# Kernel optimization log

Hardware: AMD Instinct MI355X
Metric: run time of the kernel (lower is better)

The kernel has to match this reference:

```python
import jax
jax.config.update("jax_enable_x64", True)
import jax.numpy as jnp
import numpy as np

# Paillier parameters (small primes so all modular arithmetic is exact in int64)
P, Q = 59, 61
N = P * Q                    # 3599, public modulus
N2 = N * N                   # 12,952,801; (N2-1)^2 < 2^63 -> int64-safe
LAM = (P - 1) * (Q - 1) // np.gcd(P - 1, Q - 1)   # lcm(p-1, q-1) = 870
MU = pow(int(LAM), -1, int(N))                     # lambda^{-1} mod n (g = n+1 variant)
LAM_BITS = [(LAM >> i) & 1 for i in range(int(LAM).bit_length())]  # LSB-first, static


def _decrypt(c):
    """Batched Paillier decryption: m = L(c^lambda mod n^2) * mu mod n, L(x)=(x-1)//n."""
    b = c % N2
    r = jnp.ones_like(b)
    # static square-and-multiply over the 10 bits of lambda (fully unrolled, elementwise)
    for bit in LAM_BITS:
        if bit:
            r = (r * b) % N2
        b = (b * b) % N2
    return ((r - 1) // N * MU) % N


def setup_inputs() -> dict:
    key = jax.random.key(0)
    k1, _ = jax.random.split(key)
    c = jax.random.randint(k1, (8192, 4096), 1, N2, dtype=jnp.int64)
    inv_scale = jnp.ones((1,), dtype=jnp.float32)
    return {"c": c, "inv_scale": inv_scale}


def reference(c, inv_scale):
    dec = _decrypt(c).astype(jnp.float32)
    # original: activation(decrypt(c) / 1000); inv_scale == 1.0 keeps math identical
    return jax.nn.relu(dec * (inv_scale / 1000.0))
```

## Files before the change

### kernel.cpp

```cpp
#include <hip/hip_runtime.h>
#include <stdint.h>

static constexpr uint32_t PP  = 59, QQ = 61;
static constexpr uint32_t Nn  = PP * QQ;
static constexpr uint32_t P2  = PP * PP;
static constexpr uint32_t Q2  = QQ * QQ;
static constexpr uint32_t LAM = 1740;

constexpr uint32_t cinv(uint32_t a, uint32_t m) {
    for (uint32_t x = 1; x < m; ++x) if ((uint64_t)a * x % m == 1u) return x;
    return 0u;
}
static constexpr uint32_t MU  = cinv(LAM % Nn, Nn);
static constexpr uint32_t IQP = cinv(P2 % Q2, Q2);
static constexpr uint32_t GAM = cinv(PP % QQ, QQ);
static constexpr uint32_t CPP = (cinv(QQ % PP, PP) * (MU % PP)) % PP;
static constexpr uint32_t CQQ = (cinv(PP % QQ, QQ) * (MU % QQ)) % QQ;

static constexpr int TPN = 3484;
static constexpr int TQN = 3724;
static constexpr int TT  = TPN + TQN;
static constexpr size_t WS_NEED = (size_t)TT * 4;

__device__ __forceinline__ uint32_t mul24lo(uint32_t a, uint32_t b) {
    uint32_t r;
    asm("v_mul_u32_u24 %0, %1, %2" : "=v"(r) : "v"(a), "v"(b));
    return r;
}
__device__ __forceinline__ uint32_t mul24hi(uint32_t a, uint32_t b) {
    uint32_t r;
    asm("v_mul_hi_u32_u24 %0, %1, %2" : "=v"(r) : "v"(a), "v"(b));
    return r;
}
__device__ __forceinline__ uint32_t mad24_59(uint32_t a, uint32_t c) {
    uint32_t r;
    asm("v_mad_u32_u24 %0, %1, 59, %2" : "=v"(r) : "v"(a), "v"(c));
    return r;
}

template<uint32_t D>
__device__ __forceinline__ uint32_t mod24(uint32_t x) {
    constexpr uint32_t M = (uint32_t)((1ull << 32) / D);
    uint32_t q = mul24hi(x, M);
    uint32_t r = x - mul24lo(q, D);
    return min(r, r - D);
}

template<uint32_t MOD>
__device__ uint32_t pow1740(uint32_t base) {
    uint32_t b = base % MOD, r = 1u, e = LAM;
    while (e) {
        if (e & 1u) r = (r * b) % MOD;
        b = (b * b) % MOD;
        e >>= 1u;
    }
    return r;
}
__device__ uint32_t m_from_r(uint32_t r) {
    if (r == 0u) return Nn - MU;
    uint32_t x = (r - 1u) / Nn;
    return (x * MU) % Nn;
}
__device__ uint32_t tp_entry(uint32_t i) {
    uint32_t a = pow1740<P2>(i);
    uint32_t flag = (i % PP == 0u) ? 0x80000000u : 0u;
    uint32_t gp = 0u, mp = 0u;
    if (!flag) {
        uint32_t s = (a - 1u) / PP;
        mp = (s * CPP) % PP;
        gp = (mp * GAM) % QQ;
    }
    uint32_t t = (uint32_t)(((uint64_t)((Q2 - a % Q2) % Q2) * IQP) % Q2);
    uint32_t r = a + P2 * t;
    uint32_t dq = m_from_r(r);
    return gp | (mp << 8) | (dq << 16) | flag;
}
__device__ uint32_t tq_entry(uint32_t i) {
    uint32_t b = pow1740<Q2>(i);
    uint32_t flag = (i % QQ == 0u) ? 0x80000000u : 0u;
    uint32_t gq = 0u;
    if (!flag) {
        uint32_t s = (b - 1u) / QQ;
        uint32_t mq = (s * CQQ) % QQ;
        gq = (mq * GAM) % QQ;
    }
    uint32_t t = (uint32_t)(((uint64_t)b * IQP) % Q2);
    uint32_t r = P2 * t;
    uint32_t dp = m_from_r(r);
    return gq | (dp << 16) | flag;
}

__global__ void build_tables(uint32_t* __restrict__ T) {
    int i = blockIdx.x * blockDim.x + threadIdx.x;
    if (i < TPN) T[i]       = (i < (int)P2) ? tp_entry((uint32_t)i) : 0u;
    if (i < TQN) T[TPN + i] = (i < (int)Q2) ? tq_entry((uint32_t)i) : 0u;
}

__device__ __forceinline__ float dec1(uint32_t c, const uint32_t* sTp,
                                      const uint32_t* sTq, float scale) {
    uint32_t up = sTp[mod24<P2>(c)];
    uint32_t uq = sTq[mod24<Q2>(c)];
    uint32_t gp  = up & 63u;
    uint32_t mp  = (up >> 8) & 63u;
    uint32_t dqv = (up >> 16) & 0xFFFu;
    uint32_t gq  = uq & 63u;
    uint32_t dpv = (uq >> 16) & 0xFFFu;
    uint32_t d = gq + QQ - gp;
    d = min(d, d - QQ);
    uint32_t m = mad24_59(d, mp);
    m = ((int32_t)uq < 0) ? dqv : m;
    m = ((int32_t)up < 0) ? dpv : m;
    return fmaxf((float)m * scale, 0.0f);
}

#define BLK 512

__global__ __launch_bounds__(BLK, 8) void paillier_main(
        const uint4* __restrict__ in4, float4* __restrict__ out,
        const uint32_t* __restrict__ T, const float* __restrict__ inv_scale,
        int n4) {
    __shared__ uint32_t sT[TT];
    for (int k = threadIdx.x; k < TT / 4; k += BLK)
        ((uint4*)sT)[k] = ((const uint4*)T)[k];
    __syncthreads();
    const uint32_t* sTp = sT;
    const uint32_t* sTq = sT + TPN;

    float scale = inv_scale[0] / 1000.0f;

    int stride = gridDim.x * BLK;
    for (int i = blockIdx.x * BLK + threadIdx.x; i < n4; i += stride) {
        uint4 a = in4[i];
        float4 o;
        o.x = dec1(a.x, sTp, sTq, scale);
        o.y = dec1(a.y, sTp, sTq, scale);
        o.z = dec1(a.z, sTp, sTq, scale);
        o.w = dec1(a.w, sTp, sTq, scale);
        out[i] = o;
    }
}

__global__ __launch_bounds__(BLK) void paillier_main_fb(
        const uint4* __restrict__ in4, float4* __restrict__ out,
        const float* __restrict__ inv_scale, int n4) {
    __shared__ uint32_t sT[TT];
    for (int i = threadIdx.x; i < (int)P2; i += BLK) sT[i]       = tp_entry((uint32_t)i);
    for (int i = threadIdx.x; i < (int)Q2; i += BLK) sT[TPN + i] = tq_entry((uint32_t)i);
    __syncthreads();
    const uint32_t* sTp = sT;
    const uint32_t* sTq = sT + TPN;
    float scale = inv_scale[0] / 1000.0f;
    int stride = gridDim.x * BLK;
    for (int i = blockIdx.x * BLK + threadIdx.x; i < n4; i += stride) {
        uint4 a = in4[i];
        float4 o;
        o.x = dec1(a.x, sTp, sTq, scale);
        o.y = dec1(a.y, sTp, sTq, scale);
        o.z = dec1(a.z, sTp, sTq, scale);
        o.w = dec1(a.w, sTp, sTq, scale);
        out[i] = o;
    }
}

extern "C" void kernel_launch(void* const* d_in, const int* in_sizes, int n_in,
                              void* d_out, int out_size, void* d_ws, size_t ws_size,
                              hipStream_t stream) {
    const uint4* c        = (const uint4*)d_in[0];
    const float* invscale = (const float*)d_in[1];
    float4* out           = (float4*)d_out;

    int n  = in_sizes[0];
    int n4 = n / 4;

    int nblk = 1024;
    int need = (n4 + BLK - 1) / BLK;
    if (nblk > need) nblk = need;

    if (ws_size >= WS_NEED && d_ws != nullptr) {
        uint32_t* T = (uint32_t*)d_ws;
        build_tables<<<(TQN + 255) / 256, 256, 0, stream>>>(T);
        paillier_main<<<nblk, BLK, 0, stream>>>(c, out, T, invscale, n4);
    } else {
        paillier_main_fb<<<nblk, BLK, 0, stream>>>(c, out, invscale, n4);
    }
}
```

Before: 235.3 us.

## Software-pipeline input loads four strides ahead and use nontemporal stores

The grid-stride decrypt loop is restructured so each thread holds four uint4 loads in flight and issues the next batch of four before decoding the current one. This is meant to hide global-memory latency in a bandwidth-bound streaming kernel. Output stores become nontemporal to reduce cache pollution. The extra live registers may lower occupancy under the 512x8 launch bounds.

New measurement: 240.6 us. +2.2%, slower.

```diff
diff --git a/kernel.cpp b/kernel.cpp
--- a/kernel.cpp
+++ b/kernel.cpp
@@ -113,7 +113,58 @@
     return fmaxf((float)m * scale, 0.0f);
 }
 
+__device__ __forceinline__ float4 dec4(uint4 a, const uint32_t* sTp,
+                                       const uint32_t* sTq, float scale) {
+    float4 o;
+    o.x = dec1(a.x, sTp, sTq, scale);
+    o.y = dec1(a.y, sTp, sTq, scale);
+    o.z = dec1(a.z, sTp, sTq, scale);
+    o.w = dec1(a.w, sTp, sTq, scale);
+    return o;
+}
+
+typedef float f32x4_t __attribute__((ext_vector_type(4)));
+__device__ __forceinline__ void st4(float4* __restrict__ out, int i, float4 o) {
+    f32x4_t v = {o.x, o.y, o.z, o.w};
+    __builtin_nontemporal_store(v, reinterpret_cast<f32x4_t*>(out + i));
+}
+
 #define BLK 512
+
+__device__ __forceinline__ void dec_loop(const uint4* __restrict__ in4,
+                                         float4* __restrict__ out,
+                                         const uint32_t* sTp, const uint32_t* sTq,
+                                         float scale, int n4) {
+    const int stride = gridDim.x * BLK;
+    int i = blockIdx.x * BLK + threadIdx.x;
+    if (i + 3 * stride < n4) {
+        uint4 a0 = in4[i];
+        uint4 a1 = in4[i + stride];
+        uint4 a2 = in4[i + 2 * stride];
+        uint4 a3 = in4[i + 3 * stride];
+        int j = i + 4 * stride;
+        while (j + 3 * stride < n4) {
+            uint4 b0 = in4[j];
+            uint4 b1 = in4[j + stride];
+            uint4 b2 = in4[j + 2 * stride];
+            uint4 b3 = in4[j + 3 * stride];
+            st4(out, i,              dec4(a0, sTp, sTq, scale));
+            st4(out, i + stride,     dec4(a1, sTp, sTq, scale));
+            st4(out, i + 2 * stride, dec4(a2, sTp, sTq, scale));
+            st4(out, i + 3 * stride, dec4(a3, sTp, sTq, scale));
+            a0 = b0; a1 = b1; a2 = b2; a3 = b3;
+            i = j; j += 4 * stride;
+        }
+        st4(out, i,              dec4(a0, sTp, sTq, scale));
+        st4(out, i + stride,     dec4(a1, sTp, sTq, scale));
+        st4(out, i + 2 * stride, dec4(a2, sTp, sTq, scale));
+        st4(out, i + 3 * stride, dec4(a3, sTp, sTq, scale));
+        i += 4 * stride;
+    }
+    for (; i < n4; i += stride) {
+        st4(out, i, dec4(in4[i], sTp, sTq, scale));
+    }
+}
 
 __global__ __launch_bounds__(BLK, 8) void paillier_main(
         const uint4* __restrict__ in4, float4* __restrict__ out,
@@ -127,17 +178,7 @@
     const uint32_t* sTq = sT + TPN;
 
     float scale = inv_scale[0] / 1000.0f;
-
-    int stride = gridDim.x * BLK;
-    for (int i = blockIdx.x * BLK + threadIdx.x; i < n4; i += stride) {
-        uint4 a = in4[i];
-        float4 o;
-        o.x = dec1(a.x, sTp, sTq, scale);
-        o.y = dec1(a.y, sTp, sTq, scale);
-        o.z = dec1(a.z, sTp, sTq, scale);
-        o.w = dec1(a.w, sTp, sTq, scale);
-        out[i] = o;
-    }
+    dec_loop(in4, out, sTp, sTq, scale, n4);
 }
 
 __global__ __launch_bounds__(BLK) void paillier_main_fb(
@@ -150,16 +191,7 @@
     const uint32_t* sTp = sT;
     const uint32_t* sTq = sT + TPN;
     float scale = inv_scale[0] / 1000.0f;
-    int stride = gridDim.x * BLK;
-    for (int i = blockIdx.x * BLK + threadIdx.x; i < n4; i += stride) {
-        uint4 a = in4[i];
-        float4 o;
-        o.x = dec1(a.x, sTp, sTq, scale);
-        o.y = dec1(a.y, sTp, sTq, scale);
-        o.z = dec1(a.z, sTp, sTq, scale);
-        o.w = dec1(a.w, sTp, sTq, scale);
-        out[i] = o;
-    }
+    dec_loop(in4, out, sTp, sTq, scale, n4);
 }
 
 extern "C" void kernel_launch(void* const* d_in, const int* in_sizes, int n_in,
```

## Add unrolled software-pipelined decrypt kernel with asm loads and nontemporal stores

Applied to the files above, without the earlier changes.

Adds a specialized kernel, used when the element count is exactly 16 float4 per thread across 1024 blocks. It fully unrolls the grid-stride loop and keeps four dwordx4 loads in flight, using inline asm loads and explicit vmcnt waits, so load latency overlaps the table-lookup decryption. Outputs are written with nontemporal stores to avoid polluting the cache. The cost is a shape-specific path whose hand-counted waitcnt values depend on stores also counting toward vmcnt, plus generic and fallback kernels kept for other sizes.

Result: slower. 242.9 us (+3.2%).

```diff
diff --git a/kernel.cpp b/kernel.cpp
--- a/kernel.cpp
+++ b/kernel.cpp
@@ -21,6 +21,9 @@
 static constexpr int TQN = 3724;
 static constexpr int TT  = TPN + TQN;
 static constexpr size_t WS_NEED = (size_t)TT * 4;
+
+typedef uint32_t u32x4 __attribute__((ext_vector_type(4)));
+typedef float    f32x4 __attribute__((ext_vector_type(4)));
 
 __device__ __forceinline__ uint32_t mul24lo(uint32_t a, uint32_t b) {
     uint32_t r;
@@ -113,21 +116,88 @@
     return fmaxf((float)m * scale, 0.0f);
 }
 
+__device__ __forceinline__ f32x4 dec4v(u32x4 a, const uint32_t* sTp,
+                                       const uint32_t* sTq, float scale) {
+    f32x4 o;
+    o.x = dec1(a.x, sTp, sTq, scale);
+    o.y = dec1(a.y, sTp, sTq, scale);
+    o.z = dec1(a.z, sTp, sTq, scale);
+    o.w = dec1(a.w, sTp, sTq, scale);
+    return o;
+}
+
 #define BLK 512
 
-__global__ __launch_bounds__(BLK, 8) void paillier_main(
-        const uint4* __restrict__ in4, float4* __restrict__ out,
+#define LD4(A, VOFF, BASE) \
+    asm volatile("global_load_dwordx4 %0, %1, %2" \
+                 : "=v"(A) : "v"(VOFF), "s"(BASE))
+#define ST4NT(VOFF, O, BASE) \
+    asm volatile("global_store_dwordx4 %0, %1, %2 nt" \
+                 :: "v"(VOFF), "v"(O), "s"(BASE))
+#define WAITDEP(N, A, O) \
+    asm volatile("s_waitcnt vmcnt(" #N ")" : "+v"(A), "+v"(O))
+
+#define SLOT_LD(N, A, O) do {                      \
+    WAITDEP(N, A, O);                              \
+    O = dec4v(A, sTp, sTq, scale);                 \
+    LD4(A, voff_ld, in4);  voff_ld += s16;         \
+    ST4NT(voff_st, O, out); voff_st += s16;        \
+} while (0)
+#define SLOT_NOLD(N, A, O) do {                    \
+    WAITDEP(N, A, O);                              \
+    O = dec4v(A, sTp, sTq, scale);                 \
+    ST4NT(voff_st, O, out); voff_st += s16;        \
+} while (0)
+
+__global__ __launch_bounds__(BLK, 8) void paillier_main16(
+        const uint32_t* __restrict__ in4, float* __restrict__ out,
         const uint32_t* __restrict__ T, const float* __restrict__ inv_scale,
         int n4) {
     __shared__ uint32_t sT[TT];
     for (int k = threadIdx.x; k < TT / 4; k += BLK)
         ((uint4*)sT)[k] = ((const uint4*)T)[k];
+
+    float scale = inv_scale[0] / 1000.0f;
+    asm volatile("" :: "v"(scale));
     __syncthreads();
     const uint32_t* sTp = sT;
     const uint32_t* sTq = sT + TPN;
 
-    float scale = inv_scale[0] / 1000.0f;
-
+    const uint32_t s16 = (uint32_t)(gridDim.x * BLK) * 16u;
+    uint32_t voff_ld = (uint32_t)(blockIdx.x * BLK + threadIdx.x) * 16u;
+    uint32_t voff_st = voff_ld;
+
+    u32x4 a0, a1, a2, a3;
+    f32x4 o0 = {0,0,0,0}, o1 = {0,0,0,0}, o2 = {0,0,0,0}, o3 = {0,0,0,0};
+
+    LD4(a0, voff_ld, in4); voff_ld += s16;
+    LD4(a1, voff_ld, in4); voff_ld += s16;
+    LD4(a2, voff_ld, in4); voff_ld += s16;
+    LD4(a3, voff_ld, in4); voff_ld += s16;
+
+    SLOT_LD(3, a0, o0);
+    SLOT_LD(4, a1, o1);
+    SLOT_LD(5, a2, o2);
+    SLOT_LD(6, a3, o3);
+    SLOT_LD(6, a0, o0);
+    SLOT_LD(6, a1, o1);
+    SLOT_LD(6, a2, o2);
+    SLOT_LD(6, a3, o3);
+    SLOT_LD(6, a0, o0);
+    SLOT_LD(6, a1, o1);
+    SLOT_LD(6, a2, o2);
+    SLOT_LD(6, a3, o3);
+    SLOT_NOLD(6, a0, o0);
+    SLOT_NOLD(5, a1, o1);
+    SLOT_NOLD(4, a2, o2);
+    SLOT_NOLD(3, a3, o3);
+}
+
+__device__ __forceinline__ void dec_loop_gen(const uint4* __restrict__ in4,
+                                             float4* __restrict__ out,
+                                             const uint32_t* sTp,
+                                             const uint32_t* sTq,
+                                             float scale, int n4) {
     int stride = gridDim.x * BLK;
     for (int i = blockIdx.x * BLK + threadIdx.x; i < n4; i += stride) {
         uint4 a = in4[i];
@@ -140,6 +210,18 @@
     }
 }
 
+__global__ __launch_bounds__(BLK) void paillier_main_gen(
+        const uint4* __restrict__ in4, float4* __restrict__ out,
+        const uint32_t* __restrict__ T, const float* __restrict__ inv_scale,
+        int n4) {
+    __shared__ uint32_t sT[TT];
+    for (int k = threadIdx.x; k < TT / 4; k += BLK)
+        ((uint4*)sT)[k] = ((const uint4*)T)[k];
+    __syncthreads();
+    float scale = inv_scale[0] / 1000.0f;
+    dec_loop_gen(in4, out, sT, sT + TPN, scale, n4);
+}
+
 __global__ __launch_bounds__(BLK) void paillier_main_fb(
         const uint4* __restrict__ in4, float4* __restrict__ out,
         const float* __restrict__ inv_scale, int n4) {
@@ -147,19 +229,8 @@
     for (int i = threadIdx.x; i < (int)P2; i += BLK) sT[i]       = tp_entry((uint32_t)i);
     for (int i = threadIdx.x; i < (int)Q2; i += BLK) sT[TPN + i] = tq_entry((uint32_t)i);
     __syncthreads();
-    const uint32_t* sTp = sT;
-    const uint32_t* sTq = sT + TPN;
     float scale = inv_scale[0] / 1000.0f;
-    int stride = gridDim.x * BLK;
-    for (int i = blockIdx.x * BLK + threadIdx.x; i < n4; i += stride) {
-        uint4 a = in4[i];
-        float4 o;
-        o.x = dec1(a.x, sTp, sTq, scale);
-        o.y = dec1(a.y, sTp, sTq, scale);
-        o.z = dec1(a.z, sTp, sTq, scale);
-        o.w = dec1(a.w, sTp, sTq, scale);
-        out[i] = o;
-    }
+    dec_loop_gen(in4, out, sT, sT + TPN, scale, n4);
 }
 
 extern "C" void kernel_launch(void* const* d_in, const int* in_sizes, int n_in,
@@ -176,10 +247,17 @@
     int need = (n4 + BLK - 1) / BLK;
     if (nblk > need) nblk = need;
 
+    bool exact16 = (nblk == 1024) && (n4 == 16 * nblk * BLK);
+
     if (ws_size >= WS_NEED && d_ws != nullptr) {
         uint32_t* T = (uint32_t*)d_ws;
         build_tables<<<(TQN + 255) / 256, 256, 0, stream>>>(T);
-        paillier_main<<<nblk, BLK, 0, stream>>>(c, out, T, invscale, n4);
+        if (exact16) {
+            paillier_main16<<<nblk, BLK, 0, stream>>>(
+                (const uint32_t*)c, (float*)out, T, invscale, n4);
+        } else {
+            paillier_main_gen<<<nblk, BLK, 0, stream>>>(c, out, T, invscale, n4);
+        }
     } else {
         paillier_main_fb<<<nblk, BLK, 0, stream>>>(c, out, invscale, n4);
     }
```
